# Kernel optimization log

Hardware: AMD Instinct MI355X
Metric: run time of the kernel (lower is better)

Reference implementation:

```python
import jax, jax.numpy as jnp
import numpy as np

B, T, N, D, H, C = 64, 128, 32, 64, 128, 64
LN_EPS = 1e-5


def _ln(x, g, b):
    mu = jnp.mean(x, axis=-1, keepdims=True)
    var = jnp.var(x, axis=-1, keepdims=True)
    return (x - mu) * jax.lax.rsqrt(var + LN_EPS) * g + b


def setup_inputs() -> dict:
    key = jax.random.key(0)
    ks = jax.random.split(key, 24)
    s = 0.02
    inp = {
        "embedding": jax.random.normal(ks[0], (B, T, N, D), jnp.float32),
        "context": jax.random.normal(ks[1], (B, C), jnp.float32),
        # flatten GRN: input N*D -> hidden H -> output N
        "f_Wskip": s * jax.random.normal(ks[2], (N * D, N), jnp.float32),
        "f_bskip": jnp.zeros((N,), jnp.float32),
        "f_W1": s * jax.random.normal(ks[3], (N * D, H), jnp.float32),
        "f_b1": jnp.zeros((H,), jnp.float32),
        "f_Wc": s * jax.random.normal(ks[4], (C, H), jnp.float32),
        "f_W2": s * jax.random.normal(ks[5], (H, H), jnp.float32),
        "f_b2": jnp.zeros((H,), jnp.float32),
        "f_Wg": s * jax.random.normal(ks[6], (H, 2 * N), jnp.float32),
        "f_bg": jnp.zeros((2 * N,), jnp.float32),
        "f_g": jnp.ones((N,), jnp.float32),
        "f_b": jnp.zeros((N,), jnp.float32),
        # per-variable GRNs, stacked over N: input D -> hidden H -> output H
        "v_Wskip": s * jax.random.normal(ks[7], (N, D, H), jnp.float32),
        "v_bskip": jnp.zeros((N, H), jnp.float32),
        "v_W1": s * jax.random.normal(ks[8], (N, D, H), jnp.float32),
        "v_b1": jnp.zeros((N, H), jnp.float32),
        "v_W2": s * jax.random.normal(ks[9], (N, H, H), jnp.float32),
        "v_b2": jnp.zeros((N, H), jnp.float32),
        "v_Wg": s * jax.random.normal(ks[10], (N, H, 2 * H), jnp.float32),
        "v_bg": jnp.zeros((N, 2 * H), jnp.float32),
        "v_g": jnp.ones((N, H), jnp.float32),
        "v_b": jnp.zeros((N, H), jnp.float32),
    }
    return inp


def _glu(x):
    a, b = jnp.split(x, 2, axis=-1)
    return a * jax.nn.sigmoid(b)


def reference(embedding, context,
              f_Wskip, f_bskip, f_W1, f_b1, f_Wc, f_W2, f_b2, f_Wg, f_bg, f_g, f_b,
              v_Wskip, v_bskip, v_W1, v_b1, v_W2, v_b2, v_Wg, v_bg, v_g, v_b):
    Bc, Tc, Nc, Dc = embedding.shape
    # ---- flatten GRN -> selection logits ----
    flat = embedding.reshape(Bc, Tc, Nc * Dc)               # [B,T,N*D]
    skip = flat @ f_Wskip + f_bskip                          # [B,T,N]
    h = flat @ f_W1 + f_b1 + (context @ f_Wc)[:, None, :]    # [B,T,H]
    h = jax.nn.elu(h)
    h = h @ f_W2 + f_b2                                      # [B,T,H]
    logits = _ln(_glu(h @ f_Wg + f_bg) + skip, f_g, f_b)     # [B,T,N]
    weights = jax.nn.softmax(logits, axis=-1)                # [B,T,N]
    # ---- per-variable GRNs (grouped GEMM over N) ----
    vskip = jnp.einsum('btnd,ndh->btnh', embedding, v_Wskip) + v_bskip
    vh = jnp.einsum('btnd,ndh->btnh', embedding, v_W1) + v_b1
    vh = jax.nn.elu(vh)
    vh = jnp.einsum('btnh,nhk->btnk', vh, v_W2) + v_b2
    vg = jnp.einsum('btnh,nhk->btnk', vh, v_Wg) + v_bg       # [B,T,N,2H]
    transformed = _ln(_glu(vg) + vskip, v_g, v_b)            # [B,T,N,H]
    # ---- softmax-weighted combination ----
    outputs = jnp.einsum('btn,btnh->bth', weights, transformed)
    return outputs, weights
```

## Files before the change

kernel.cpp:

```cpp
#include <hip/hip_runtime.h>
#include <hip/hip_bf16.h>

#define TOK   8192
#define NVAR  32
#define DDIM  64
#define HDIM  128
#define CDIM  64
#define ND    2048
#define LN_EPS 1e-5f
#define TTV   32

typedef float f32x4 __attribute__((ext_vector_type(4)));
typedef short s16x8 __attribute__((ext_vector_type(8)));
typedef unsigned short u16x8 __attribute__((ext_vector_type(8)));

__device__ __forceinline__ float bf2f(unsigned short u) {
    unsigned int x = ((unsigned int)u) << 16;
    return __uint_as_float(x);
}
__device__ __forceinline__ unsigned short f2bf(float f) {
    unsigned int x = __float_as_uint(f);
    unsigned int r = (x + 0x7fffu + ((x >> 16) & 1u)) >> 16;
    return (unsigned short)r;
}
__device__ __forceinline__ float elu_f(float x) {
    return x > 0.f ? x : (__expf(x) - 1.f);
}
__device__ __forceinline__ float sigm_f(float x) {
    return 1.f / (1.f + __expf(-x));
}
__device__ __forceinline__ s16x8 frag_ld(const unsigned short* p) {
    return __builtin_bit_cast(s16x8, *(const u16x8*)p);
}
__device__ __forceinline__ f32x4 mfma_bf16(s16x8 a, s16x8 b, f32x4 c) {
    return __builtin_amdgcn_mfma_f32_16x16x32_bf16(a, b, c, 0, 0, 0);
}

__global__ __launch_bounds__(256) void k_pack_all(
        const float* __restrict__ vW1, const float* __restrict__ vWsk,
        const float* __restrict__ vW2, const float* __restrict__ vWg,
        const float* __restrict__ fW1, const float* __restrict__ fWsk,
        const float* __restrict__ fW2, const float* __restrict__ fWg,
        unsigned short* __restrict__ pk1, unsigned short* __restrict__ pksk,
        unsigned short* __restrict__ pk2, unsigned short* __restrict__ pkg,
        unsigned short* __restrict__ pfW1, unsigned short* __restrict__ pfWsk,
        unsigned short* __restrict__ pfW2, unsigned short* __restrict__ pfWg) {
    int sg = blockIdx.x * 4 + (threadIdx.x >> 6);
    int lane = threadIdx.x & 63;
    const float* W; unsigned short* out; int K, N, NF, n, bx;
    if (sg < 512)       {                 W = vW1;  out = pk1;  K = 64;   N = 128; NF = 8;  n = sg >> 4;  bx = sg & 15; }
    else if (sg < 1024) { int i = sg - 512;  W = vWsk; out = pksk; K = 64;   N = 128; NF = 8;  n = i >> 4; bx = i & 15; }
    else if (sg < 2048) { int i = sg - 1024; W = vW2;  out = pk2;  K = 128;  N = 128; NF = 8;  n = i >> 5; bx = i & 31; }
    else if (sg < 4096) { int i = sg - 2048; W = vWg;  out = pkg;  K = 128;  N = 256; NF = 16; n = i >> 6; bx = i & 63; }
    else if (sg < 4608) { int i = sg - 4096; W = fW1;  out = pfW1; K = 2048; N = 128; NF = 8;  n = 0;      bx = i; }
    else if (sg < 4736) { int i = sg - 4608; W = fWsk; out = pfWsk; K = 2048; N = 32; NF = 2;  n = 0;      bx = i; }
    else if (sg < 4768) { int i = sg - 4736; W = fW2;  out = pfW2; K = 128;  N = 128; NF = 8;  n = 0;      bx = i; }
    else                { int i = sg - 4768; W = fWg;  out = pfWg; K = 128;  N = 64;  NF = 4;  n = 0;      bx = i; }
    int ks = bx / NF, nf = bx - ks * NF;
    int col = nf * 16 + (lane & 15);
    int k0 = ks * 32 + (lane >> 4) * 8;
    const float* src = W + (size_t)n * K * N + (size_t)k0 * N + col;
    unsigned short* dst = out + (size_t)n * K * N + ((size_t)bx * 64 + lane) * 8;
    unsigned short v[8];
#pragma unroll
    for (int j = 0; j < 8; ++j) v[j] = f2bf(src[(size_t)j * N]);
    *(u16x8*)dst = *(const u16x8*)v;
}

__global__ __launch_bounds__(128) void k_fsel(const float* __restrict__ emb,
        const float* __restrict__ ctx, const float* __restrict__ fWc,
        const unsigned short* __restrict__ pfW1, const unsigned short* __restrict__ pfWsk,
        const float* __restrict__ fb1, const float* __restrict__ fbsk,
        const unsigned short* __restrict__ pfW2, const float* __restrict__ fb2,
        const unsigned short* __restrict__ pfWg, const float* __restrict__ fbg,
        const float* __restrict__ fg, const float* __restrict__ fb,
        float* __restrict__ wout) {
    __shared__ __align__(16) unsigned short pool[11136];
    float* CTX = (float*)pool;
    unsigned short* H1 = pool + 256;
    unsigned short* H2 = pool + 4608;
    float* SK = (float*)(pool + 8960);
    float* G  = (float*)(pool + 256);

    const int tid = threadIdx.x;
    const int lane = tid & 63, w = tid >> 6, lr = lane & 15, lk = lane >> 4;
    const int tok0 = blockIdx.x * 32;
    const int b = tok0 >> 7;

    {
        float acc = 0.f;
        const float* cr = ctx + b * CDIM;
#pragma unroll 8
        for (int c = 0; c < CDIM; ++c) acc += cr[c] * fWc[c * HDIM + tid];
        CTX[tid] = acc;
    }

    const float* arow = emb + (size_t)(tok0 + w * 16 + lr) * ND + lk * 8;
    f32x4 acc[10] = {};
    for (int ks = 0; ks < 64; ++ks) {
        float4 a0 = *(const float4*)(arow + ks * 32);
        float4 a1 = *(const float4*)(arow + ks * 32 + 4);
        unsigned short av[8];
        av[0] = f2bf(a0.x); av[1] = f2bf(a0.y); av[2] = f2bf(a0.z); av[3] = f2bf(a0.w);
        av[4] = f2bf(a1.x); av[5] = f2bf(a1.y); av[6] = f2bf(a1.z); av[7] = f2bf(a1.w);
        s16x8 af = __builtin_bit_cast(s16x8, *(u16x8*)av);
#pragma unroll
        for (int nf = 0; nf < 8; ++nf) {
            s16x8 bf = frag_ld(pfW1 + ((size_t)(ks * 8 + nf) * 64 + lane) * 8);
            acc[nf] = mfma_bf16(af, bf, acc[nf]);
        }
#pragma unroll
        for (int nf = 0; nf < 2; ++nf) {
            s16x8 bf = frag_ld(pfWsk + ((size_t)(ks * 2 + nf) * 64 + lane) * 8);
            acc[8 + nf] = mfma_bf16(af, bf, acc[8 + nf]);
        }
    }
    __syncthreads();

#pragma unroll
    for (int nf = 0; nf < 8; ++nf) {
        int col = nf * 16 + lr;
        float add = fb1[col] + CTX[col];
#pragma unroll
        for (int r = 0; r < 4; ++r)
            H1[(w * 16 + lk * 4 + r) * 136 + col] = f2bf(elu_f(acc[nf][r] + add));
    }
#pragma unroll
    for (int nf = 0; nf < 2; ++nf) {
        int col = nf * 16 + lr;
        float add = fbsk[col];
#pragma unroll
        for (int r = 0; r < 4; ++r)
            SK[(w * 16 + lk * 4 + r) * 34 + col] = acc[8 + nf][r] + add;
    }
    __syncthreads();

    {
        f32x4 a2[8] = {};
#pragma unroll
        for (int ks = 0; ks < 4; ++ks) {
            s16x8 af = frag_ld(H1 + (w * 16 + lr) * 136 + ks * 32 + lk * 8);
#pragma unroll
            for (int nf = 0; nf < 8; ++nf) {
                s16x8 bf = frag_ld(pfW2 + ((size_t)(ks * 8 + nf) * 64 + lane) * 8);
                a2[nf] = mfma_bf16(af, bf, a2[nf]);
            }
        }
#pragma unroll
        for (int nf = 0; nf < 8; ++nf) {
            int col = nf * 16 + lr;
            float add = fb2[col];
#pragma unroll
            for (int r = 0; r < 4; ++r)
                H2[(w * 16 + lk * 4 + r) * 136 + col] = f2bf(a2[nf][r] + add);
        }
    }
    __syncthreads();

    {
        f32x4 a3[4] = {};
#pragma unroll
        for (int ks = 0; ks < 4; ++ks) {
            s16x8 af = frag_ld(H2 + (w * 16 + lr) * 136 + ks * 32 + lk * 8);
#pragma unroll
            for (int nf = 0; nf < 4; ++nf) {
                s16x8 bf = frag_ld(pfWg + ((size_t)(ks * 4 + nf) * 64 + lane) * 8);
                a3[nf] = mfma_bf16(af, bf, a3[nf]);
            }
        }
#pragma unroll
        for (int nf = 0; nf < 4; ++nf) {
            int col = nf * 16 + lr;
            float add = fbg[col];
#pragma unroll
            for (int r = 0; r < 4; ++r)
                G[(w * 16 + lk * 4 + r) * 68 + col] = a3[nf][r] + add;
        }
    }
    __syncthreads();

    {
        int grp = tid >> 5, t = tid & 31;
        float fgv = fg[t], fbv = fb[t];
#pragma unroll 2
        for (int j = 0; j < 8; ++j) {
            int tr = grp * 8 + j;
            float a = G[tr * 68 + t];
            float bb = G[tr * 68 + 32 + t];
            float val = a * sigm_f(bb) + SK[tr * 34 + t];
            float s = val, q = val * val;
#pragma unroll
            for (int m = 16; m >= 1; m >>= 1) { s += __shfl_xor(s, m, 32); q += __shfl_xor(q, m, 32); }
            float mean = s * (1.f / 32.f);
            float var = q * (1.f / 32.f) - mean * mean;
            float logit = (val - mean) * rsqrtf(var + LN_EPS) * fgv + fbv;
            float mx = logit;
#pragma unroll
            for (int m = 16; m >= 1; m >>= 1) mx = fmaxf(mx, __shfl_xor(mx, m, 32));
            float e = __expf(logit - mx);
            float se = e;
#pragma unroll
            for (int m = 16; m >= 1; m >>= 1) se += __shfl_xor(se, m, 32);
            wout[(size_t)(tok0 + tr) * NVAR + t] = e / se;
        }
    }
}

__global__ __launch_bounds__(256, 2) void k_var(
        const float* __restrict__ emb,
        const unsigned short* __restrict__ pk1, const unsigned short* __restrict__ pksk,
        const unsigned short* __restrict__ pk2, const unsigned short* __restrict__ pkg,
        const float* __restrict__ vb1, const float* __restrict__ vbsk,
        const float* __restrict__ vb2, const float* __restrict__ vbg,
        const float* __restrict__ gam, const float* __restrict__ bet,
        const float* __restrict__ wsel, float* __restrict__ outp) {
    __shared__ __align__(16) unsigned short pool[7296];
    unsigned short* EB  = pool;
    unsigned short* VHB = pool + 2304;
    float* LNp = (float*)(pool + 6656);
    float* LNm = (float*)(pool + 7168);

    const int tid = threadIdx.x;
    const int lane = tid & 63;
    const int w = tid >> 6;
    const int lr = lane & 15;
    const int lk = lane >> 4;
    const int tok0 = blockIdx.x * TTV;
    const int gbase = blockIdx.y * 8;

    const int prow = tid >> 3, pc0 = (tid & 7) * 8;

    float accO[2][2][4] = {};

    {
        const float* src = emb + ((size_t)(tok0 + prow) * NVAR + gbase) * DDIM + pc0;
        unsigned short* dst = EB + prow * 72 + pc0;
#pragma unroll
        for (int q = 0; q < 2; ++q) {
            float4 v = *(const float4*)(src + q * 4);
            ushort4 t;
            t.x = f2bf(v.x); t.y = f2bf(v.y); t.z = f2bf(v.z); t.w = f2bf(v.w);
            *(ushort4*)(dst + q * 4) = t;
        }
    }
    __syncthreads();

    for (int nn = 0; nn < 8; ++nn) {
        const int n = gbase + nn;

        f32x4 c2[2][2];
#pragma unroll
        for (int mf = 0; mf < 2; ++mf)
#pragma unroll
            for (int nf = 0; nf < 2; ++nf) c2[mf][nf] = (f32x4){0.f, 0.f, 0.f, 0.f};
        {
            f32x4 c1[2][2] = {};
#pragma unroll
            for (int ks = 0; ks < 2; ++ks) {
                s16x8 af[2];
#pragma unroll
                for (int mf = 0; mf < 2; ++mf)
                    af[mf] = frag_ld(EB + (mf * 16 + lr) * 72 + ks * 32 + lk * 8);
                const unsigned short* p1 = pk1 + (size_t)n * 8192 + ((size_t)(ks * 8 + w * 2) * 64 + lane) * 8;
                const unsigned short* ps = pksk + (size_t)n * 8192 + ((size_t)(ks * 8 + w * 2) * 64 + lane) * 8;
                s16x8 b10 = frag_ld(p1), b11 = frag_ld(p1 + 512);
                s16x8 bs0 = frag_ld(ps), bs1 = frag_ld(ps + 512);
#pragma unroll
                for (int mf = 0; mf < 2; ++mf) {
                    c1[mf][0] = mfma_bf16(af[mf], b10, c1[mf][0]);
                    c1[mf][1] = mfma_bf16(af[mf], b11, c1[mf][1]);
                    c2[mf][0] = mfma_bf16(af[mf], bs0, c2[mf][0]);
                    c2[mf][1] = mfma_bf16(af[mf], bs1, c2[mf][1]);
                }
            }
#pragma unroll
            for (int nf = 0; nf < 2; ++nf) {
                int col = w * 32 + nf * 16 + lr;
                float bb1 = vb1[n * HDIM + col];
                float bbs = vbsk[n * HDIM + col];
#pragma unroll
                for (int mf = 0; mf < 2; ++mf) {
                    c2[mf][nf] = c2[mf][nf] + bbs;
#pragma unroll
                    for (int r = 0; r < 4; ++r)
                        VHB[(mf * 16 + lk * 4 + r) * 136 + col] = f2bf(elu_f(c1[mf][nf][r] + bb1));
                }
            }
        }
        __syncthreads();

        float4 pf0, pf1;
        if (nn < 7) {
            const float* src = emb + ((size_t)(tok0 + prow) * NVAR + n + 1) * DDIM + pc0;
            pf0 = *(const float4*)(src);
            pf1 = *(const float4*)(src + 4);
        }

        f32x4 c3[2][2] = {};
        {
#pragma unroll
            for (int ks = 0; ks < 4; ++ks) {
                s16x8 af[2];
#pragma unroll
                for (int mf = 0; mf < 2; ++mf)
                    af[mf] = frag_ld(VHB + (mf * 16 + lr) * 136 + ks * 32 + lk * 8);
                const unsigned short* p2 = pk2 + (size_t)n * 16384 + ((size_t)(ks * 8 + w * 2) * 64 + lane) * 8;
                s16x8 b0 = frag_ld(p2), b1 = frag_ld(p2 + 512);
#pragma unroll
                for (int mf = 0; mf < 2; ++mf) {
                    c3[mf][0] = mfma_bf16(af[mf], b0, c3[mf][0]);
                    c3[mf][1] = mfma_bf16(af[mf], b1, c3[mf][1]);
                }
            }
        }
        __syncthreads();

        {
#pragma unroll
            for (int nf = 0; nf < 2; ++nf) {
                int col = w * 32 + nf * 16 + lr;
                float bb = vb2[n * HDIM + col];
#pragma unroll
                for (int mf = 0; mf < 2; ++mf)
#pragma unroll
                    for (int r = 0; r < 4; ++r)
                        VHB[(mf * 16 + lk * 4 + r) * 136 + col] = f2bf(c3[mf][nf][r] + bb);
            }
            if (nn < 7) {
                unsigned short* dst = EB + prow * 72 + pc0;
                ushort4 t;
                t.x = f2bf(pf0.x); t.y = f2bf(pf0.y); t.z = f2bf(pf0.z); t.w = f2bf(pf0.w);
                *(ushort4*)(dst) = t;
                t.x = f2bf(pf1.x); t.y = f2bf(pf1.y); t.z = f2bf(pf1.z); t.w = f2bf(pf1.w);
                *(ushort4*)(dst + 4) = t;
            }
        }
        __syncthreads();

        float vv[2][2][4];
        float s_[2][4], q_[2][4];
        {
            f32x4 c4[2][4] = {};
#pragma unroll
            for (int ks = 0; ks < 4; ++ks) {
                s16x8 af[2];
#pragma unroll
                for (int mf = 0; mf < 2; ++mf)
                    af[mf] = frag_ld(VHB + (mf * 16 + lr) * 136 + ks * 32 + lk * 8);
                const unsigned short* pg = pkg + (size_t)n * 32768;
                s16x8 ba0 = frag_ld(pg + ((size_t)(ks * 16 + 2 * w + 0) * 64 + lane) * 8);
                s16x8 ba1 = frag_ld(pg + ((size_t)(ks * 16 + 2 * w + 1) * 64 + lane) * 8);
                s16x8 bb0 = frag_ld(pg + ((size_t)(ks * 16 + 2 * w + 8) * 64 + lane) * 8);
                s16x8 bb1 = frag_ld(pg + ((size_t)(ks * 16 + 2 * w + 9) * 64 + lane) * 8);
#pragma unroll
                for (int mf = 0; mf < 2; ++mf) {
                    c4[mf][0] = mfma_bf16(af[mf], ba0, c4[mf][0]);
                    c4[mf][1] = mfma_bf16(af[mf], ba1, c4[mf][1]);
                    c4[mf][2] = mfma_bf16(af[mf], bb0, c4[mf][2]);
                    c4[mf][3] = mfma_bf16(af[mf], bb1, c4[mf][3]);
                }
            }
            float bga0 = vbg[n * 256 + w * 32 + lr];
            float bga1 = vbg[n * 256 + w * 32 + 16 + lr];
            float bgb0 = vbg[n * 256 + 128 + w * 32 + lr];
            float bgb1 = vbg[n * 256 + 128 + w * 32 + 16 + lr];
#pragma unroll
            for (int mf = 0; mf < 2; ++mf)
#pragma unroll
                for (int r = 0; r < 4; ++r) {
                    float a0 = c4[mf][0][r] + bga0;
                    float b0 = c4[mf][2][r] + bgb0;
                    float x0 = a0 * sigm_f(b0) + c2[mf][0][r];
                    float a1 = c4[mf][1][r] + bga1;
                    float b1 = c4[mf][3][r] + bgb1;
                    float x1 = a1 * sigm_f(b1) + c2[mf][1][r];
                    vv[mf][0][r] = x0; vv[mf][1][r] = x1;
                    s_[mf][r] = x0 + x1;
                    q_[mf][r] = x0 * x0 + x1 * x1;
                }
#pragma unroll
            for (int mf = 0; mf < 2; ++mf)
#pragma unroll
                for (int r = 0; r < 4; ++r) {
#pragma unroll
                    for (int m = 1; m < 16; m <<= 1) {
                        s_[mf][r] += __shfl_xor(s_[mf][r], m);
                        q_[mf][r] += __shfl_xor(q_[mf][r], m);
                    }
                }
            if (lr == 0) {
#pragma unroll
                for (int mf = 0; mf < 2; ++mf)
#pragma unroll
                    for (int r = 0; r < 4; ++r) {
                        int row = mf * 16 + lk * 4 + r;
                        LNp[row * 8 + w * 2] = s_[mf][r];
                        LNp[row * 8 + w * 2 + 1] = q_[mf][r];
                    }
            }
        }
        __syncthreads();

        if (tid < 128) {
            int row = tid >> 2, p = tid & 3;
            float ss = LNp[row * 8 + p * 2];
            float qq = LNp[row * 8 + p * 2 + 1];
            ss += __shfl_xor(ss, 1); qq += __shfl_xor(qq, 1);
            ss += __shfl_xor(ss, 2); qq += __shfl_xor(qq, 2);
            if (p == 0) {
                float mean = ss * (1.f / 128.f);
                float var = qq * (1.f / 128.f) - mean * mean;
                LNm[row * 2] = mean;
                LNm[row * 2 + 1] = rsqrtf(var + LN_EPS);
            }
        }
        __syncthreads();

        {
            float ga0 = gam[n * HDIM + w * 32 + lr];
            float ga1 = gam[n * HDIM + w * 32 + 16 + lr];
            float be0 = bet[n * HDIM + w * 32 + lr];
            float be1 = bet[n * HDIM + w * 32 + 16 + lr];
#pragma unroll
            for (int mf = 0; mf < 2; ++mf)
#pragma unroll
                for (int r = 0; r < 4; ++r) {
                    int row = mf * 16 + lk * 4 + r;
                    float mean = LNm[row * 2], inv = LNm[row * 2 + 1];
                    float wgt = wsel[(size_t)(tok0 + row) * NVAR + n];
                    accO[mf][0][r] += wgt * ((vv[mf][0][r] - mean) * inv * ga0 + be0);
                    accO[mf][1][r] += wgt * ((vv[mf][1][r] - mean) * inv * ga1 + be1);
                }
        }
    }

    {
#pragma unroll
        for (int mf = 0; mf < 2; ++mf)
#pragma unroll
            for (int r = 0; r < 4; ++r) {
                int row = mf * 16 + lk * 4 + r;
                float* po = outp + (size_t)(tok0 + row) * HDIM + w * 32 + lr;
                atomicAdd(po, accO[mf][0][r]);
                atomicAdd(po + 16, accO[mf][1][r]);
            }
    }
}

extern "C" void kernel_launch(void* const* d_in, const int* in_sizes, int n_in,
                              void* d_out, int out_size, void* d_ws, size_t ws_size,
                              hipStream_t stream) {
    const float* emb  = (const float*)d_in[0];
    const float* ctx  = (const float*)d_in[1];
    const float* fWsk = (const float*)d_in[2];
    const float* fbsk = (const float*)d_in[3];
    const float* fW1  = (const float*)d_in[4];
    const float* fb1  = (const float*)d_in[5];
    const float* fWc  = (const float*)d_in[6];
    const float* fW2  = (const float*)d_in[7];
    const float* fb2  = (const float*)d_in[8];
    const float* fWg  = (const float*)d_in[9];
    const float* fbg  = (const float*)d_in[10];
    const float* fg   = (const float*)d_in[11];
    const float* fb   = (const float*)d_in[12];
    const float* vWsk = (const float*)d_in[13];
    const float* vbsk = (const float*)d_in[14];
    const float* vW1  = (const float*)d_in[15];
    const float* vb1  = (const float*)d_in[16];
    const float* vW2  = (const float*)d_in[17];
    const float* vb2  = (const float*)d_in[18];
    const float* vWg  = (const float*)d_in[19];
    const float* vbg  = (const float*)d_in[20];
    const float* vgam = (const float*)d_in[21];
    const float* vbet = (const float*)d_in[22];

    float* outp = (float*)d_out;
    float* wout = outp + (size_t)TOK * HDIM;

    unsigned short* pk1  = (unsigned short*)d_ws;
    unsigned short* pksk = pk1 + 262144;
    unsigned short* pk2  = pksk + 262144;
    unsigned short* pkg  = pk2 + 524288;
    unsigned short* pfW1 = pkg + 1048576;
    unsigned short* pfWsk= pfW1 + 262144;
    unsigned short* pfW2 = pfWsk + 65536;
    unsigned short* pfWg = pfW2 + 16384;

    hipMemsetAsync(d_out, 0, (size_t)TOK * HDIM * sizeof(float), stream);
    k_pack_all<<<1196, 256, 0, stream>>>(vW1, vWsk, vW2, vWg, fW1, fWsk, fW2, fWg,
                                         pk1, pksk, pk2, pkg, pfW1, pfWsk, pfW2, pfWg);
    k_fsel<<<256, 128, 0, stream>>>(emb, ctx, fWc, pfW1, pfWsk, fb1, fbsk,
                                    pfW2, fb2, pfWg, fbg, fg, fb, wout);
    k_var<<<dim3(TOK / TTV, 4), 256, 0, stream>>>(emb, pk1, pksk, pk2, pkg,
                                                  vb1, vbsk, vb2, vbg, vgam, vbet,
                                                  wout, outp);
}
```

Measured before the change: 173.7 us.

## Split-K the flatten GRN GEMM across four waves in k_fsel

Doubles k_fsel's block size to 256 threads and splits the K=2048 reduction of the first flatten GEMM across two wave pairs. Each pair handles half of K, and the partial accumulators are summed through shared memory. This halves the serial K loop per wave, which matters because the grid has only 256 blocks on a large GPU. The cost is more LDS use, an extra reduction pass and barrier, and half the threads sitting idle during the later small GEMMs and softmax.

```diff
diff --git a/kernel.cpp b/kernel.cpp
--- a/kernel.cpp
+++ b/kernel.cpp
@@ -67,7 +67,7 @@
     *(u16x8*)dst = *(const u16x8*)v;
 }
 
-__global__ __launch_bounds__(128) void k_fsel(const float* __restrict__ emb,
+__global__ __launch_bounds__(256) void k_fsel(const float* __restrict__ emb,
         const float* __restrict__ ctx, const float* __restrict__ fWc,
         const unsigned short* __restrict__ pfW1, const unsigned short* __restrict__ pfWsk,
         const float* __restrict__ fb1, const float* __restrict__ fbsk,
@@ -75,29 +75,35 @@
         const unsigned short* __restrict__ pfWg, const float* __restrict__ fbg,
         const float* __restrict__ fg, const float* __restrict__ fb,
         float* __restrict__ wout) {
-    __shared__ __align__(16) unsigned short pool[11136];
+    __shared__ __align__(16) unsigned short pool[21376];
     float* CTX = (float*)pool;
-    unsigned short* H1 = pool + 256;
-    unsigned short* H2 = pool + 4608;
-    float* SK = (float*)(pool + 8960);
-    float* G  = (float*)(pool + 256);
+    float* PRT = (float*)(pool + 256);
+    unsigned short* H1 = pool + 10496;
+    unsigned short* H2 = pool + 14848;
+    float* SK = (float*)(pool + 19200);
+    float* G  = (float*)(pool + 10496);
 
     const int tid = threadIdx.x;
-    const int lane = tid & 63, w = tid >> 6, lr = lane & 15, lk = lane >> 4;
+    const int lane = tid & 63;
+    const int w4 = tid >> 6;
+    const int mh = w4 & 1;
+    const int kh = w4 >> 1;
+    const int lr = lane & 15, lk = lane >> 4;
     const int tok0 = blockIdx.x * 32;
     const int b = tok0 >> 7;
 
-    {
-        float acc = 0.f;
+    if (tid < 128) {
+        float acc0 = 0.f;
         const float* cr = ctx + b * CDIM;
 #pragma unroll 8
-        for (int c = 0; c < CDIM; ++c) acc += cr[c] * fWc[c * HDIM + tid];
-        CTX[tid] = acc;
-    }
-
-    const float* arow = emb + (size_t)(tok0 + w * 16 + lr) * ND + lk * 8;
+        for (int c = 0; c < CDIM; ++c) acc0 += cr[c] * fWc[c * HDIM + tid];
+        CTX[tid] = acc0;
+    }
+
+    const float* arow = emb + (size_t)(tok0 + mh * 16 + lr) * ND + kh * 1024 + lk * 8;
     f32x4 acc[10] = {};
-    for (int ks = 0; ks < 64; ++ks) {
+    for (int ks = 0; ks < 32; ++ks) {
+        const int ksg = kh * 32 + ks;
         float4 a0 = *(const float4*)(arow + ks * 32);
         float4 a1 = *(const float4*)(arow + ks * 32 + 4);
         unsigned short av[8];
@@ -106,36 +112,48 @@
         s16x8 af = __builtin_bit_cast(s16x8, *(u16x8*)av);
 #pragma unroll
         for (int nf = 0; nf < 8; ++nf) {
-            s16x8 bf = frag_ld(pfW1 + ((size_t)(ks * 8 + nf) * 64 + lane) * 8);
+            s16x8 bf = frag_ld(pfW1 + ((size_t)(ksg * 8 + nf) * 64 + lane) * 8);
             acc[nf] = mfma_bf16(af, bf, acc[nf]);
         }
 #pragma unroll
         for (int nf = 0; nf < 2; ++nf) {
-            s16x8 bf = frag_ld(pfWsk + ((size_t)(ks * 2 + nf) * 64 + lane) * 8);
+            s16x8 bf = frag_ld(pfWsk + ((size_t)(ksg * 2 + nf) * 64 + lane) * 8);
             acc[8 + nf] = mfma_bf16(af, bf, acc[8 + nf]);
         }
     }
+
+    if (w4 >= 2) {
+        float* p = PRT + ((size_t)mh * 64 + lane) * 40;
+#pragma unroll
+        for (int f = 0; f < 10; ++f) *(f32x4*)(p + f * 4) = acc[f];
+    }
     __syncthreads();
-
-#pragma unroll
-    for (int nf = 0; nf < 8; ++nf) {
-        int col = nf * 16 + lr;
-        float add = fb1[col] + CTX[col];
-#pragma unroll
-        for (int r = 0; r < 4; ++r)
-            H1[(w * 16 + lk * 4 + r) * 136 + col] = f2bf(elu_f(acc[nf][r] + add));
-    }
-#pragma unroll
-    for (int nf = 0; nf < 2; ++nf) {
-        int col = nf * 16 + lr;
-        float add = fbsk[col];
-#pragma unroll
-        for (int r = 0; r < 4; ++r)
-            SK[(w * 16 + lk * 4 + r) * 34 + col] = acc[8 + nf][r] + add;
+    if (w4 < 2) {
+        const float* p = PRT + ((size_t)mh * 64 + lane) * 40;
+#pragma unroll
+        for (int f = 0; f < 10; ++f) acc[f] = acc[f] + *(const f32x4*)(p + f * 4);
+
+#pragma unroll
+        for (int nf = 0; nf < 8; ++nf) {
+            int col = nf * 16 + lr;
+            float add = fb1[col] + CTX[col];
+#pragma unroll
+            for (int r = 0; r < 4; ++r)
+                H1[(mh * 16 + lk * 4 + r) * 136 + col] = f2bf(elu_f(acc[nf][r] + add));
+        }
+#pragma unroll
+        for (int nf = 0; nf < 2; ++nf) {
+            int col = nf * 16 + lr;
+            float add = fbsk[col];
+#pragma unroll
+            for (int r = 0; r < 4; ++r)
+                SK[(mh * 16 + lk * 4 + r) * 34 + col] = acc[8 + nf][r] + add;
+        }
     }
     __syncthreads();
 
-    {
+    if (tid < 128) {
+        const int w = w4;
         f32x4 a2[8] = {};
 #pragma unroll
         for (int ks = 0; ks < 4; ++ks) {
@@ -157,7 +175,8 @@
     }
     __syncthreads();
 
-    {
+    if (tid < 128) {
+        const int w = w4;
         f32x4 a3[4] = {};
 #pragma unroll
         for (int ks = 0; ks < 4; ++ks) {
@@ -179,7 +198,7 @@
     }
     __syncthreads();
 
-    {
+    if (tid < 128) {
         int grp = tid >> 5, t = tid & 31;
         float fgv = fg[t], fbv = fb[t];
 #pragma unroll 2
@@ -489,7 +508,7 @@
     hipMemsetAsync(d_out, 0, (size_t)TOK * HDIM * sizeof(float), stream);
     k_pack_all<<<1196, 256, 0, stream>>>(vW1, vWsk, vW2, vWg, fW1, fWsk, fW2, fWg,
                                          pk1, pksk, pk2, pkg, pfW1, pfWsk, pfW2, pfWg);
-    k_fsel<<<256, 128, 0, stream>>>(emb, ctx, fWc, pfW1, pfWsk, fb1, fbsk,
+    k_fsel<<<256, 256, 0, stream>>>(emb, ctx, fWc, pfW1, pfWsk, fb1, fbsk,
                                     pfW2, fb2, pfWg, fbg, fg, fb, wout);
     k_var<<<dim3(TOK / TTV, 4), 256, 0, stream>>>(emb, pk1, pksk, pk2, pkg,
                                                   vb1, vbsk, vb2, vbg, vgam, vbet,
```

Measured after the change: 158.3 us. 1.1x faster.
